# Optimization experiments

Measured on AMD Instinct MI355X. Metric: run time of the kernel, lower is better.

Reference implementation:

```python
import jax, jax.numpy as jnp
import numpy as np
import math


def setup_inputs() -> dict:
    key = jax.random.key(0)
    k1, k2, k3 = jax.random.split(key, 3)
    img = jax.random.normal(k1, (32, 3, 512, 512), dtype=jnp.float32)
    c_u = jax.random.normal(k2, (100, 100), dtype=jnp.float32)  # scalar-field mode coeffs for dx
    c_v = jax.random.normal(k3, (100, 100), dtype=jnp.float32)  # scalar-field mode coeffs for dy
    return {"img": img, "c_u": c_u, "c_v": c_v}


def _scalar_field(c, n):
    # random scalar field of size n x n from the first m modes (m = c.shape[0])
    m = c.shape[0]
    x = jnp.linspace(0.0, 1.0, n, dtype=c.dtype)            # [n]
    k = jnp.arange(1, m + 1, dtype=c.dtype)                 # [m]
    i, j = jnp.meshgrid(k, k, indexing='ij')                # [m, m]
    r = jnp.sqrt(i ** 2 + j ** 2)
    e = (r < m + 0.5).astype(c.dtype) / r                   # sqrt(1/energy) per mode
    s = jnp.sin(jnp.pi * x[:, None] * k[None, :])           # [n, m]
    return jnp.einsum('ij,xi,yj->yx', c * e, s, s)          # [n, n]


def reference(img, c_u, c_v):
    n = img.shape[-1]  # square image assumed (n x n)
    m = c_u.shape[0]   # frequency cutoff `cut`

    # temperature_range(n, cut), deterministic T = midpoint of allowed range (alpha=1)
    log_cut = math.log(m + 1e-06)
    T1 = 1.0 / (math.pi * n ** 2 * log_cut)
    T2 = 4.0 / (math.pi ** 3 * m ** 2 * log_cut)
    T2 = max(T1, T2)
    T = 0.5 * (T1 + T2)

    # displacement fields [n, n]
    dx = (T ** 0.5) * _scalar_field(c_u, n) * n
    dy = (T ** 0.5) * _scalar_field(c_v, n) * n

    # remap with bilinear ('linear') interpolation
    dtype = dx.dtype
    y, x = jnp.meshgrid(jnp.arange(n, dtype=dtype), jnp.arange(n, dtype=dtype), indexing='ij')
    xn = jnp.clip(x - dx, 0.0, n - 1)
    yn = jnp.clip(y - dy, 0.0, n - 1)

    xf = jnp.floor(xn).astype(jnp.int32)
    yf = jnp.floor(yn).astype(jnp.int32)
    xc = jnp.ceil(xn).astype(jnp.int32)
    yc = jnp.ceil(yn).astype(jnp.int32)
    xv = xn - xf.astype(dtype)
    yv = yn - yf.astype(dtype)

    out = ((1 - yv) * (1 - xv) * img[..., yf, xf]
           + (1 - yv) * xv * img[..., yf, xc]
           + yv * (1 - xv) * img[..., yc, xf]
           + yv * xv * img[..., yc, xc])
    return out
```

## Files before the change

kernel.cpp:

```cpp
#include <hip/hip_runtime.h>
#include <math.h>

#define NN 512
#define MM 100
#define TPB 256
#define ROWS_OUT 4
#define ROWS_LDS 13
#define PLANES_PER_BLOCK 8

typedef float f32x2 __attribute__((ext_vector_type(2)));
typedef unsigned int u32;
typedef u32 u32x2 __attribute__((ext_vector_type(2)));
typedef u32 u32x4 __attribute__((ext_vector_type(4)));


__global__ void bcoef_kernel(const float* __restrict__ c_u,
                             const float* __restrict__ c_v,
                             float* __restrict__ B_u,
                             float* __restrict__ B_v) {
    __shared__ float sSt[MM];
    int x = blockIdx.x;
    int j = threadIdx.x;
    if (j < MM) {
        double arg = M_PI * ((double)x / (double)(NN - 1)) * (double)(j + 1);
        sSt[j] = (float)sin(arg);
    }
    __syncthreads();
    if (j >= MM) return;
    float au = 0.f, av = 0.f;
    for (int i = 0; i < MM; ++i) {
        int i1 = i + 1, j1 = j + 1;
        int r2i = i1 * i1 + j1 * j1;
        float w = (r2i <= 10100) ? (1.0f / sqrtf((float)r2i)) : 0.0f;
        float sw = sSt[i] * w;
        au += sw * c_u[i * MM + j];
        av += sw * c_v[i * MM + j];
    }
    B_u[j * NN + x] = au;
    B_v[j * NN + x] = av;
}

__global__ __launch_bounds__(256)
void field_weights_kernel(const float* __restrict__ B_u,
                          const float* __restrict__ B_v,
                          float scale,
                          u32x2* __restrict__ pk,
                          int* __restrict__ strip_tab) {
    __shared__ float sS[ROWS_OUT * MM];
    __shared__ int s_mn[4], s_mx[4];
    int t = threadIdx.x;
    int strip = blockIdx.x;
    int y0 = strip * ROWS_OUT;

    for (int i = t; i < ROWS_OUT * MM; i += 256) {
        int r = i / MM, j = i % MM;
        double arg = M_PI * ((double)(y0 + r) / (double)(NN - 1)) * (double)(j + 1);
        sS[i] = (float)sin(arg);
    }
    __syncthreads();

    float au[ROWS_OUT][2] = {}, av[ROWS_OUT][2] = {};
    for (int j = 0; j < MM; ++j) {
        float bu0 = B_u[j * NN + t], bu1 = B_u[j * NN + t + 256];
        float bv0 = B_v[j * NN + t], bv1 = B_v[j * NN + t + 256];
        #pragma unroll
        for (int r = 0; r < ROWS_OUT; ++r) {
            float s = sS[r * MM + j];
            au[r][0] += bu0 * s; au[r][1] += bu1 * s;
            av[r][0] += bv0 * s; av[r][1] += bv1 * s;
        }
    }

    float xvq[8], yvq[8];
    int offA[8], offB[8];
    int myf = NN, Myc = -1;
    #pragma unroll
    for (int i = 0; i < 8; ++i) {
        int c = i & 1, r = i >> 1;
        int xi = (c << 8) + t;
        int yi = y0 + r;
        float xn = fminf(fmaxf((float)xi - scale * au[r][c], 0.0f), (float)(NN - 1));
        float yn = fminf(fmaxf((float)yi - scale * av[r][c], 0.0f), (float)(NN - 1));
        int xf = (int)floorf(xn), yf = (int)floorf(yn);
        int yc = (int)ceilf(yn);
        xvq[i] = xn - (float)xf;
        yvq[i] = yn - (float)yf;
        offA[i] = (yf << 9) + xf;
        offB[i] = (yc << 9) + xf;
        myf = min(myf, yf);
        Myc = max(Myc, yc);
    }

    for (int d = 32; d; d >>= 1) {
        myf = min(myf, __shfl_xor(myf, d));
        Myc = max(Myc, __shfl_xor(Myc, d));
    }
    int wid = t >> 6;
    if ((t & 63) == 0) { s_mn[wid] = myf; s_mx[wid] = Myc; }
    __syncthreads();
    int r0 = min(min(s_mn[0], s_mn[1]), min(s_mn[2], s_mn[3]));
    int nr = max(max(s_mx[0], s_mx[1]), max(s_mx[2], s_mx[3])) - r0 + 1;
    if (t == 0) { strip_tab[2 * strip] = r0; strip_tab[2 * strip + 1] = nr; }

    int rb = r0 << 9;
    #pragma unroll
    for (int i = 0; i < 8; ++i) {
        int pix = ((y0 + (i >> 1)) << 9) + ((i & 1) << 8) + t;
        u32 oa = (u32)(offA[i] - rb);
        u32 ob = (u32)(offB[i] - rb);
        u32 xq = (u32)__float2int_rn(xvq[i] * 65535.0f);
        u32 yq = (u32)__float2int_rn(yvq[i] * 65535.0f);
        u32x2 v; v[0] = oa | (ob << 16); v[1] = xq | (yq << 16);
        pk[pix] = v;
    }
}

__global__ __launch_bounds__(TPB, 3)
void remap_kernel(const float* __restrict__ img,
                  const u32x2* __restrict__ pk,
                  const int* __restrict__ strip_tab,
                  float* __restrict__ out,
                  int planes) {
    __shared__ __align__(16) float rows[2][ROWS_LDS * NN + 4];

    int nb = gridDim.x;
    int bid = blockIdx.x;
    int sid = (bid & 7) * (nb >> 3) + (bid >> 3);
    int pg    = sid >> 7;
    int strip = sid & 127;

    int t = threadIdx.x;
    int r0 = strip_tab[2 * strip];
    int nr = strip_tab[2 * strip + 1];
    int base = ((strip * ROWS_OUT) << 9) + (t << 1);

    const u32x4* __restrict__ pk4 = (const u32x4*)pk;
    u32x4 pr[ROWS_OUT];
    #pragma unroll
    for (int r = 0; r < ROWS_OUT; ++r) pr[r] = pk4[(base + (r << 9)) >> 1];

    int p0 = pg * PLANES_PER_BLOCK;
    int p1 = p0 + PLANES_PER_BLOCK; if (p1 > planes) p1 = planes;
    const float qs = 1.0f / 65535.0f;

    if (nr <= ROWS_LDS) {
        if (t == 0) { rows[0][nr * NN] = 0.f; rows[1][nr * NN] = 0.f; }

        int nbytes = nr << 11;
        int wave = t >> 6;
        int lane_goff = t * 16;
        size_t rbo = (size_t)(r0 << 9);

        {
            const char* ipc = (const char*)(img + (size_t)p0 * (NN * NN) + rbo);
            for (int ob = 0; ob < nbytes; ob += TPB * 16) {
                if (ob + wave * 1024 < nbytes) {
                    __builtin_amdgcn_global_load_lds(
                        (const __attribute__((address_space(1))) void*)(ipc + ob + lane_goff),
                        (__attribute__((address_space(3))) void*)((char*)rows[0] + ob + wave * 1024),
                        16, 0, 0);
                }
            }
        }
        __syncthreads();

        int cur = 0;
        for (int p = p0; p < p1; ++p) {
            if (p + 1 < p1) {
                const char* ipc = (const char*)(img + (size_t)(p + 1) * (NN * NN) + rbo);
                for (int ob = 0; ob < nbytes; ob += TPB * 16) {
                    if (ob + wave * 1024 < nbytes) {
                        __builtin_amdgcn_global_load_lds(
                            (const __attribute__((address_space(1))) void*)(ipc + ob + lane_goff),
                            (__attribute__((address_space(3))) void*)((char*)rows[cur ^ 1] + ob + wave * 1024),
                            16, 0, 0);
                    }
                }
            }

            const float* __restrict__ rw = rows[cur];
            float* __restrict__ op = out + (size_t)p * (NN * NN);
            #pragma unroll
            for (int r = 0; r < ROWS_OUT; ++r) {
                u32x4 pp = pr[r];
                int oA0 = (int)(pp[0] & 0xFFFFu), oB0 = (int)(pp[0] >> 16);
                float xv0 = (float)(pp[1] & 0xFFFFu) * qs;
                float yv0 = (float)(pp[1] >> 16) * qs;
                int oA1 = (int)(pp[2] & 0xFFFFu), oB1 = (int)(pp[2] >> 16);
                float xv1 = (float)(pp[3] & 0xFFFFu) * qs;
                float yv1 = (float)(pp[3] >> 16) * qs;
                float t0 = (1.f - xv0) * rw[oA0] + xv0 * rw[oA0 + 1];
                float b0 = (1.f - xv0) * rw[oB0] + xv0 * rw[oB0 + 1];
                float t1 = (1.f - xv1) * rw[oA1] + xv1 * rw[oA1 + 1];
                float b1 = (1.f - xv1) * rw[oB1] + xv1 * rw[oB1 + 1];
                f32x2 o;
                o[0] = (1.f - yv0) * t0 + yv0 * b0;
                o[1] = (1.f - yv1) * t1 + yv1 * b1;
                __builtin_nontemporal_store(o, (f32x2*)(op + base + (r << 9)));
            }
            __syncthreads();
            cur ^= 1;
        }
    } else {
        int rb = r0 << 9;
        for (int p = p0; p < p1; ++p) {
            const float* __restrict__ ip = img + (size_t)p * (NN * NN);
            float* __restrict__ op = out + (size_t)p * (NN * NN);
            #pragma unroll
            for (int r = 0; r < ROWS_OUT; ++r) {
                u32x4 pp = pr[r];
                int a0 = (int)(pp[0] & 0xFFFFu) + rb, b0i = (int)(pp[0] >> 16) + rb;
                float xv0 = (float)(pp[1] & 0xFFFFu) * qs;
                float yv0 = (float)(pp[1] >> 16) * qs;
                int a1 = (int)(pp[2] & 0xFFFFu) + rb, b1i = (int)(pp[2] >> 16) + rb;
                float xv1 = (float)(pp[3] & 0xFFFFu) * qs;
                float yv1 = (float)(pp[3] >> 16) * qs;
                int e0 = ((a0 & 511) == 511) ? 0 : 1;
                int e1 = ((a1 & 511) == 511) ? 0 : 1;
                float t0 = (1.f - xv0) * ip[a0] + xv0 * ip[a0 + e0];
                float bo0 = (1.f - xv0) * ip[b0i] + xv0 * ip[b0i + e0];
                float t1 = (1.f - xv1) * ip[a1] + xv1 * ip[a1 + e1];
                float bo1 = (1.f - xv1) * ip[b1i] + xv1 * ip[b1i + e1];
                f32x2 o;
                o[0] = (1.f - yv0) * t0 + yv0 * bo0;
                o[1] = (1.f - yv1) * t1 + yv1 * bo1;
                __builtin_nontemporal_store(o, (f32x2*)(op + base + (r << 9)));
            }
        }
    }
}

extern "C" void kernel_launch(void* const* d_in, const int* in_sizes, int n_in,
                              void* d_out, int out_size, void* d_ws, size_t ws_size,
                              hipStream_t stream) {
    const float* img = (const float*)d_in[0];
    const float* c_u = (const float*)d_in[1];
    const float* c_v = (const float*)d_in[2];
    float* out = (float*)d_out;

    int planes = in_sizes[0] / (NN * NN);

    float* ws   = (float*)d_ws;
    float* B_u  = ws;
    float* B_v  = B_u + MM * NN;
    u32x2* pk   = (u32x2*)(ws + 2 * MM * NN);
    int* strip_tab = (int*)(ws + 2 * MM * NN + 2 * NN * NN);

    double log_cut = log((double)MM + 1e-6);
    double T1 = 1.0 / (M_PI * (double)NN * (double)NN * log_cut);
    double T2 = 4.0 / (M_PI * M_PI * M_PI * (double)MM * (double)MM * log_cut);
    if (T2 < T1) T2 = T1;
    double T = 0.5 * (T1 + T2);
    float scale = (float)(sqrt(T) * (double)NN);

    bcoef_kernel<<<NN, 128, 0, stream>>>(c_u, c_v, B_u, B_v);
    field_weights_kernel<<<NN / ROWS_OUT, 256, 0, stream>>>(B_u, B_v, scale,
                                                            pk, strip_tab);

    int strips = NN / ROWS_OUT;
    int groups = (planes + PLANES_PER_BLOCK - 1) / PLANES_PER_BLOCK;
    remap_kernel<<<strips * groups, TPB, 0, stream>>>(img, pk, strip_tab,
                                                      out, planes);
}
```

Baseline: 76.92 us.

## Stage fixed-size LDS row window with counted vmcnt waits instead of full syncthreads

The setup kernel now clamps the strip start row so every LDS strip loads a fixed ROWS_LDS rows. The remap kernel issues a fixed, unrolled sequence of 7 global_load_lds ops per plane, sending the unused slots to a scratch LDS buffer. The current plane then waits with s_waitcnt vmcnt(7) and a raw s_barrier, so the prefetch of the next plane stays in flight instead of being drained by __syncthreads. This relies on the hand-counted vmcnt matching the compiler's output and on nontemporal stores not disturbing the counter, and it loads extra rows for short strips.

```diff
diff --git a/kernel.cpp b/kernel.cpp
--- a/kernel.cpp
+++ b/kernel.cpp
@@ -99,10 +99,12 @@
     if ((t & 63) == 0) { s_mn[wid] = myf; s_mx[wid] = Myc; }
     __syncthreads();
     int r0 = min(min(s_mn[0], s_mn[1]), min(s_mn[2], s_mn[3]));
-    int nr = max(max(s_mx[0], s_mx[1]), max(s_mx[2], s_mx[3])) - r0 + 1;
-    if (t == 0) { strip_tab[2 * strip] = r0; strip_tab[2 * strip + 1] = nr; }
-
-    int rb = r0 << 9;
+    int Mc = max(max(s_mx[0], s_mx[1]), max(s_mx[2], s_mx[3]));
+    int r0c = min(r0, NN - ROWS_LDS);
+    int nrc = Mc - r0c + 1;
+    if (t == 0) { strip_tab[2 * strip] = r0c; strip_tab[2 * strip + 1] = nrc; }
+
+    int rb = r0c << 9;
     #pragma unroll
     for (int i = 0; i < 8; ++i) {
         int pix = ((y0 + (i >> 1)) << 9) + ((i & 1) << 8) + t;
@@ -122,6 +124,7 @@
                   float* __restrict__ out,
                   int planes) {
     __shared__ __align__(16) float rows[2][ROWS_LDS * NN + 4];
+    __shared__ __align__(16) float scratch[256];
 
     int nb = gridDim.x;
     int bid = blockIdx.x;
@@ -130,6 +133,8 @@
     int strip = sid & 127;
 
     int t = threadIdx.x;
+    int wave = t >> 6;
+    int lane16 = (t & 63) * 16;
     int r0 = strip_tab[2 * strip];
     int nr = strip_tab[2 * strip + 1];
     int base = ((strip * ROWS_OUT) << 9) + (t << 1);
@@ -142,41 +147,39 @@
     int p0 = pg * PLANES_PER_BLOCK;
     int p1 = p0 + PLANES_PER_BLOCK; if (p1 > planes) p1 = planes;
     const float qs = 1.0f / 65535.0f;
+    size_t rbo = (size_t)(r0 << 9);
+
+    auto STAGE = [&](float* dstbuf, const char* ipc) {
+        #pragma unroll
+        for (int it = 0; it < 7; ++it) {
+            int obase = it * 4096 + wave * 1024;
+            bool ok = obase < (ROWS_LDS << 11);
+            int gb = ok ? obase : 0;
+            char* ldst = ok ? ((char*)dstbuf + obase) : (char*)scratch;
+            __builtin_amdgcn_global_load_lds(
+                (const __attribute__((address_space(1))) void*)(ipc + gb + lane16),
+                (__attribute__((address_space(3))) void*)ldst,
+                16, 0, 0);
+        }
+    };
 
     if (nr <= ROWS_LDS) {
-        if (t == 0) { rows[0][nr * NN] = 0.f; rows[1][nr * NN] = 0.f; }
-
-        int nbytes = nr << 11;
-        int wave = t >> 6;
-        int lane_goff = t * 16;
-        size_t rbo = (size_t)(r0 << 9);
-
-        {
-            const char* ipc = (const char*)(img + (size_t)p0 * (NN * NN) + rbo);
-            for (int ob = 0; ob < nbytes; ob += TPB * 16) {
-                if (ob + wave * 1024 < nbytes) {
-                    __builtin_amdgcn_global_load_lds(
-                        (const __attribute__((address_space(1))) void*)(ipc + ob + lane_goff),
-                        (__attribute__((address_space(3))) void*)((char*)rows[0] + ob + wave * 1024),
-                        16, 0, 0);
-                }
-            }
-        }
-        __syncthreads();
+        if (t == 0) { rows[0][ROWS_LDS * NN] = 0.f; rows[1][ROWS_LDS * NN] = 0.f; }
+
+        STAGE(rows[0], (const char*)(img + (size_t)p0 * (NN * NN) + rbo));
+        asm volatile("s_waitcnt vmcnt(0)" ::: "memory");
+        __builtin_amdgcn_s_barrier();
 
         int cur = 0;
         for (int p = p0; p < p1; ++p) {
             if (p + 1 < p1) {
-                const char* ipc = (const char*)(img + (size_t)(p + 1) * (NN * NN) + rbo);
-                for (int ob = 0; ob < nbytes; ob += TPB * 16) {
-                    if (ob + wave * 1024 < nbytes) {
-                        __builtin_amdgcn_global_load_lds(
-                            (const __attribute__((address_space(1))) void*)(ipc + ob + lane_goff),
-                            (__attribute__((address_space(3))) void*)((char*)rows[cur ^ 1] + ob + wave * 1024),
-                            16, 0, 0);
-                    }
-                }
+                STAGE(rows[cur ^ 1],
+                      (const char*)(img + (size_t)(p + 1) * (NN * NN) + rbo));
+                asm volatile("s_waitcnt vmcnt(7)" ::: "memory");
+            } else {
+                asm volatile("s_waitcnt vmcnt(0)" ::: "memory");
             }
+            __builtin_amdgcn_s_barrier();
 
             const float* __restrict__ rw = rows[cur];
             float* __restrict__ op = out + (size_t)p * (NN * NN);
@@ -198,7 +201,7 @@
                 o[1] = (1.f - yv1) * t1 + yv1 * b1;
                 __builtin_nontemporal_store(o, (f32x2*)(op + base + (r << 9)));
             }
-            __syncthreads();
+            __builtin_amdgcn_s_barrier();
             cur ^= 1;
         }
     } else {
```

Result: slower. 79.74 us (+3.7%).

## Fuse coefficient contraction into field kernel with sine recurrence for x modes

Applied to the files above, without the earlier changes.

Removes the separate bcoef kernel and its B_u/B_v workspace round trip. Each strip block now contracts the coefficient matrices against its own y-sine rows in shared memory first. It then accumulates over modes, generating sin(k*theta_x) with a double-precision Chebyshev recurrence instead of loading precomputed B values. This saves one launch and global traffic but repeats the 100x100 contraction in every block. The recurrence can drift in accuracy slightly.

```diff
diff --git a/kernel.cpp b/kernel.cpp
--- a/kernel.cpp
+++ b/kernel.cpp
@@ -13,61 +13,69 @@
 typedef u32 u32x2 __attribute__((ext_vector_type(2)));
 typedef u32 u32x4 __attribute__((ext_vector_type(4)));
 
-
-__global__ void bcoef_kernel(const float* __restrict__ c_u,
-                             const float* __restrict__ c_v,
-                             float* __restrict__ B_u,
-                             float* __restrict__ B_v) {
-    __shared__ float sSt[MM];
-    int x = blockIdx.x;
-    int j = threadIdx.x;
-    if (j < MM) {
-        double arg = M_PI * ((double)x / (double)(NN - 1)) * (double)(j + 1);
-        sSt[j] = (float)sin(arg);
-    }
-    __syncthreads();
-    if (j >= MM) return;
-    float au = 0.f, av = 0.f;
-    for (int i = 0; i < MM; ++i) {
-        int i1 = i + 1, j1 = j + 1;
-        int r2i = i1 * i1 + j1 * j1;
-        float w = (r2i <= 10100) ? (1.0f / sqrtf((float)r2i)) : 0.0f;
-        float sw = sSt[i] * w;
-        au += sw * c_u[i * MM + j];
-        av += sw * c_v[i * MM + j];
-    }
-    B_u[j * NN + x] = au;
-    B_v[j * NN + x] = av;
-}
+#define AS1 __attribute__((address_space(1)))
+#define AS3 __attribute__((address_space(3)))
+
 
 __global__ __launch_bounds__(256)
-void field_weights_kernel(const float* __restrict__ B_u,
-                          const float* __restrict__ B_v,
+void field_weights_kernel(const float* __restrict__ c_u,
+                          const float* __restrict__ c_v,
                           float scale,
                           u32x2* __restrict__ pk,
                           int* __restrict__ strip_tab) {
-    __shared__ float sS[ROWS_OUT * MM];
+    __shared__ float sy[ROWS_OUT * MM];
+    __shared__ float Au[ROWS_OUT * MM], Av[ROWS_OUT * MM];
     __shared__ int s_mn[4], s_mx[4];
     int t = threadIdx.x;
     int strip = blockIdx.x;
     int y0 = strip * ROWS_OUT;
 
-    for (int i = t; i < ROWS_OUT * MM; i += 256) {
-        int r = i / MM, j = i % MM;
+    for (int idx = t; idx < ROWS_OUT * MM; idx += 256) {
+        int r = idx / MM, j = idx % MM;
         double arg = M_PI * ((double)(y0 + r) / (double)(NN - 1)) * (double)(j + 1);
-        sS[i] = (float)sin(arg);
+        sy[idx] = (float)sin(arg);
     }
     __syncthreads();
 
-    float au[ROWS_OUT][2] = {}, av[ROWS_OUT][2] = {};
-    for (int j = 0; j < MM; ++j) {
-        float bu0 = B_u[j * NN + t], bu1 = B_u[j * NN + t + 256];
-        float bv0 = B_v[j * NN + t], bv1 = B_v[j * NN + t + 256];
+    for (int idx = t; idx < 2 * ROWS_OUT * MM; idx += 256) {
+        int f = idx >= ROWS_OUT * MM;
+        int rem = f ? idx - ROWS_OUT * MM : idx;
+        int r = rem & 3, i = rem >> 2;
+        const float* __restrict__ cf = f ? c_v : c_u;
+        int i1 = i + 1;
+        float acc = 0.f;
+        for (int j = 0; j < MM; ++j) {
+            int j1 = j + 1;
+            int r2i = i1 * i1 + j1 * j1;
+            float w = (r2i <= 10100) ? (1.0f / sqrtf((float)r2i)) : 0.0f;
+            acc += cf[i * MM + j] * w * sy[r * MM + j];
+        }
+        (f ? Av : Au)[r * MM + i] = acc;
+    }
+    __syncthreads();
+
+    float au[2][ROWS_OUT] = {}, av[2][ROWS_OUT] = {};
+    double s_cur[2], s_prev[2], c2[2];
+    #pragma unroll
+    for (int c = 0; c < 2; ++c) {
+        int x = t + (c << 8);
+        double th = M_PI * ((double)x / (double)(NN - 1));
+        c2[c] = 2.0 * cos(th);
+        s_prev[c] = 0.0;
+        s_cur[c] = sin(th);
+    }
+    for (int i = 0; i < MM; ++i) {
+        float A0u = Au[i], A1u = Au[MM + i], A2u = Au[2 * MM + i], A3u = Au[3 * MM + i];
+        float A0v = Av[i], A1v = Av[MM + i], A2v = Av[2 * MM + i], A3v = Av[3 * MM + i];
         #pragma unroll
-        for (int r = 0; r < ROWS_OUT; ++r) {
-            float s = sS[r * MM + j];
-            au[r][0] += bu0 * s; au[r][1] += bu1 * s;
-            av[r][0] += bv0 * s; av[r][1] += bv1 * s;
+        for (int c = 0; c < 2; ++c) {
+            float sx = (float)s_cur[c];
+            au[c][0] += A0u * sx; au[c][1] += A1u * sx;
+            au[c][2] += A2u * sx; au[c][3] += A3u * sx;
+            av[c][0] += A0v * sx; av[c][1] += A1v * sx;
+            av[c][2] += A2v * sx; av[c][3] += A3v * sx;
+            double nxt = c2[c] * s_cur[c] - s_prev[c];
+            s_prev[c] = s_cur[c]; s_cur[c] = nxt;
         }
     }
 
@@ -79,8 +87,8 @@
         int c = i & 1, r = i >> 1;
         int xi = (c << 8) + t;
         int yi = y0 + r;
-        float xn = fminf(fmaxf((float)xi - scale * au[r][c], 0.0f), (float)(NN - 1));
-        float yn = fminf(fmaxf((float)yi - scale * av[r][c], 0.0f), (float)(NN - 1));
+        float xn = fminf(fmaxf((float)xi - scale * au[c][r], 0.0f), (float)(NN - 1));
+        float yn = fminf(fmaxf((float)yi - scale * av[c][r], 0.0f), (float)(NN - 1));
         int xf = (int)floorf(xn), yf = (int)floorf(yn);
         int yc = (int)ceilf(yn);
         xvq[i] = xn - (float)xf;
@@ -156,9 +164,8 @@
             for (int ob = 0; ob < nbytes; ob += TPB * 16) {
                 if (ob + wave * 1024 < nbytes) {
                     __builtin_amdgcn_global_load_lds(
-                        (const __attribute__((address_space(1))) void*)(ipc + ob + lane_goff),
-                        (__attribute__((address_space(3))) void*)((char*)rows[0] + ob + wave * 1024),
-                        16, 0, 0);
+                        (const AS1 void*)(ipc + ob + lane_goff),
+                        (AS3 void*)((char*)rows[0] + ob + wave * 1024), 16, 0, 0);
                 }
             }
         }
@@ -171,9 +178,8 @@
                 for (int ob = 0; ob < nbytes; ob += TPB * 16) {
                     if (ob + wave * 1024 < nbytes) {
                         __builtin_amdgcn_global_load_lds(
-                            (const __attribute__((address_space(1))) void*)(ipc + ob + lane_goff),
-                            (__attribute__((address_space(3))) void*)((char*)rows[cur ^ 1] + ob + wave * 1024),
-                            16, 0, 0);
+                            (const AS1 void*)(ipc + ob + lane_goff),
+                            (AS3 void*)((char*)rows[cur ^ 1] + ob + wave * 1024), 16, 0, 0);
                     }
                 }
             }
@@ -241,10 +247,8 @@
     int planes = in_sizes[0] / (NN * NN);
 
     float* ws   = (float*)d_ws;
-    float* B_u  = ws;
-    float* B_v  = B_u + MM * NN;
-    u32x2* pk   = (u32x2*)(ws + 2 * MM * NN);
-    int* strip_tab = (int*)(ws + 2 * MM * NN + 2 * NN * NN);
+    u32x2* pk   = (u32x2*)ws;
+    int* strip_tab = (int*)(ws + 2 * NN * NN);
 
     double log_cut = log((double)MM + 1e-6);
     double T1 = 1.0 / (M_PI * (double)NN * (double)NN * log_cut);
@@ -253,8 +257,7 @@
     double T = 0.5 * (T1 + T2);
     float scale = (float)(sqrt(T) * (double)NN);
 
-    bcoef_kernel<<<NN, 128, 0, stream>>>(c_u, c_v, B_u, B_v);
-    field_weights_kernel<<<NN / ROWS_OUT, 256, 0, stream>>>(B_u, B_v, scale,
+    field_weights_kernel<<<NN / ROWS_OUT, 256, 0, stream>>>(c_u, c_v, scale,
                                                             pk, strip_tab);
 
     int strips = NN / ROWS_OUT;
```

Measured after the change: 88.10 us. 14.5% more time.
